# Kernel tuning notes

Measured on AMD Instinct MI355X. Metric: run time of the kernel, lower is better.

The kernel has to match this reference:

```python
import jax, jax.numpy as jnp
import numpy as np

N, L, N_KNOTS = 512, 64, 9
N_BINS = N_KNOTS - 1
TWO_PI = 2.0 * np.pi


def _circular_conv(x, w, b):
    # x: (N,C,H,W), w: (O,C,3,3); circular (periodic) padding as used for gauge lattices
    xp = jnp.pad(x, ((0, 0), (0, 0), (1, 1), (1, 1)), mode='wrap')
    y = jax.lax.conv_general_dilated(xp, w, (1, 1), 'VALID',
                                     dimension_numbers=('NCHW', 'OIHW', 'NCHW'))
    return y + b[None, :, None, None]


def setup_inputs() -> dict:
    key = jax.random.key(0)
    k1, k2, k3 = jax.random.split(key, 3)
    x = jax.random.normal(k1, (N, L, L), dtype=jnp.float32)
    # partition the lattice into active/passive/frozen masks
    pat = (np.add.outer(np.arange(L), 2 * np.arange(L)) % 3)
    mask_active = jnp.asarray((pat == 0).astype(np.float32))
    mask_passive = jnp.asarray((pat == 1).astype(np.float32))
    mask_frozen = jnp.asarray((pat == 2).astype(np.float32))
    conv1_w = 0.1 * jax.random.normal(k2, (32, 2, 3, 3), dtype=jnp.float32)
    conv1_b = jnp.zeros((32,), jnp.float32)
    conv2_w = 0.1 * jax.random.normal(k3, (3 * N_BINS + 1, 32, 3, 3), dtype=jnp.float32)
    conv2_b = jnp.zeros((3 * N_BINS + 1,), jnp.float32)
    return {"x": x, "mask_active": mask_active, "mask_passive": mask_passive,
            "mask_frozen": mask_frozen, "conv1_w": conv1_w, "conv1_b": conv1_b,
            "conv2_w": conv2_w, "conv2_b": conv2_b}


def reference(x, mask_active, mask_passive, mask_frozen, conv1_w, conv1_b, conv2_w, conv2_b):
    nb = N_BINS
    # prepare_u1_input: frozen-masked (cos, sin) channels
    net_in = mask_frozen[None, None] * jnp.stack([jnp.cos(x), jnp.sin(x)], axis=1)  # (N,2,L,L)
    h1 = jax.nn.gelu(_circular_conv(net_in, conv1_w, conv1_b))
    net_out = _circular_conv(h1, conv2_w, conv2_b)              # (N,3nb+1,L,L)
    net_out = jnp.transpose(net_out, (0, 2, 3, 1))              # (N,L,L,3nb+1)
    w = jax.nn.softmax(net_out[..., :nb], axis=-1)
    h = jax.nn.softmax(net_out[..., nb:2 * nb], axis=-1)
    d = jax.nn.softplus(net_out[..., 2 * nb:3 * nb])
    t = net_out[..., -1]
    # circular knots on [0, 2pi]; periodic derivative: s[-1] = s[0]
    zeros = jnp.zeros(w.shape[:-1] + (1,), w.dtype)
    kx = jnp.concatenate([zeros, TWO_PI * jnp.cumsum(w, -1)], -1)   # (N,L,L,n_knots)
    ky = jnp.concatenate([zeros, TWO_PI * jnp.cumsum(h, -1)], -1)
    s = jnp.concatenate([d, d[..., :1]], -1)
    # dir = 0 (forward): x1 = active * mod(x)
    x1 = mask_active[None] * jnp.remainder(x, TWO_PI)
    # bin search over interior knots -> k in [0, nb-1]
    k = jnp.sum((x1[..., None] >= kx[..., 1:-1]).astype(jnp.int32), axis=-1)
    g = lambda a, i: jnp.take_along_axis(a, i[..., None], axis=-1)[..., 0]
    kxk, kxk1 = g(kx, k), g(kx, k + 1)
    kyk, kyk1 = g(ky, k), g(ky, k + 1)
    sk, sk1 = g(s, k), g(s, k + 1)
    wk = kxk1 - kxk
    hk = kyk1 - kyk
    slope = hk / wk
    xi = jnp.clip((x1 - kxk) / wk, 0.0, 1.0)
    om = 1.0 - xi
    # rational-quadratic spline (Durkan et al. 2019)
    den = slope + (sk1 + sk - 2.0 * slope) * xi * om
    y = kyk + hk * (slope * xi * xi + sk * xi * om) / den
    local_logJ = jnp.log(slope * slope * (sk1 * xi * xi + 2.0 * slope * xi * om + sk * om * om)) \
                 - 2.0 * jnp.log(den)
    fx1 = mask_active[None] * (y + t)              # (1-dir)*t with dir=0
    local_logJ = mask_active[None] * local_logJ
    logJ = jnp.sum(local_logJ, axis=(1, 2))
    fx = mask_active[None] * jnp.remainder(fx1, TWO_PI) + mask_passive[None] * x + mask_frozen[None] * x
    return fx, logJ
```

## Files before the change

kernel.cpp:

```cpp
#include <hip/hip_runtime.h>
#include <math.h>

#define Nn 512
#define Ld 64
#define NB 8
#define C1 32
#define C2 25
#define CHUNK 8

#define ICOLS 68
#define ISTR  69
#define IROWSMAX 16
#define HCOLS 66
#define HSTR  67
#define HPLANE 945

__device__ __forceinline__ float gelu_tanh(float a) {
    float a3 = a * a * a;
    float t = tanhf(0.7978845608028654f * (a + 0.044715f * a3));
    return 0.5f * a * (1.0f + t);
}

__device__ __forceinline__ float softplus_f(float v) {
    return (v > 0.0f) ? v + log1pf(expf(-v)) : log1pf(expf(v));
}

__device__ __forceinline__ float pos_mod_2pi(float v) {
    const float T = 6.2831853071795864769f;
    float r = fmodf(v, T);
    if (r < 0.0f) r += T;
    return r;
}

__global__ __launch_bounds__(256, 4) void csplaq_v4_kernel(
    const float* __restrict__ x,
    const float* __restrict__ c1w, const float* __restrict__ c1b,
    const float* __restrict__ c2w, const float* __restrict__ c2b,
    float* __restrict__ out_fx, float* __restrict__ out_logJ)
{
    __shared__ float s_cos[IROWSMAX * ISTR];
    __shared__ float s_sin[IROWSMAX * ISTR];
    __shared__ float s_h1[CHUNK * HPLANE];
    __shared__ float s_red[4];

    const float TWO_PI_F = 6.2831853071795864769f;

    const int tid  = threadIdx.x;
    const int band = blockIdx.x;
    const int n    = blockIdx.y;
    const int r0   = band * 12;
    const int R    = (band == 5) ? 4 : 12;
    const int rows_in  = R + 4;
    const int nsite_h  = (R + 2) * HCOLS;
    const int n_active = (R == 12) ? 256 : 86;
    const float* xn = x + n * Ld * Ld;

    for (int idx = tid; idx < rows_in * ICOLS; idx += 256) {
        int li = idx / ICOLS, uu = idx - li * ICOLS;
        int gi = (r0 - 2 + li) & 63;
        int gj = (uu - 2) & 63;
        float xv = xn[gi * Ld + gj];
        int pat = (gi + 2 * gj) % 3;
        float sv, cv;
        sincosf(xv, &sv, &cv);
        float fz = (pat == 2) ? 1.0f : 0.0f;
        s_cos[li * ISTR + uu] = fz * cv;
        s_sin[li * ISTR + uu] = fz * sv;
    }

    int g3 = tid >> 6, u = tid & 63;
    int rsel  = (u >= 22) + (u >= 43);
    int ubase = (rsel == 2) ? 43 : ((rsel == 1) ? 22 : 0);
    int rr = 3 * g3 + rsel;
    int cc = 3 * (u - ubase) + rsel;
    bool is_act = (tid < n_active);

    float acc[C2];
    #pragma unroll
    for (int co = 0; co < C2; ++co) acc[co] = c2b[co];

    for (int c0 = 0; c0 < C1; c0 += CHUNK) {
        __syncthreads();
        for (int s = tid; s < nsite_h; s += 256) {
            int h = s / HCOLS, j = s - h * HCOLS;
            float v[18];
            #pragma unroll
            for (int di = 0; di < 3; ++di)
                #pragma unroll
                for (int dj = 0; dj < 3; ++dj) {
                    int a = (h + di) * ISTR + (j + dj);
                    v[di * 3 + dj]     = s_cos[a];
                    v[9 + di * 3 + dj] = s_sin[a];
                }
            #pragma unroll
            for (int c = 0; c < CHUNK; ++c) {
                const float* w = c1w + (c0 + c) * 18;
                float a1 = c1b[c0 + c];
                #pragma unroll
                for (int t = 0; t < 9; ++t) {
                    a1 = fmaf(v[t],     w[t],     a1);
                    a1 = fmaf(v[9 + t], w[9 + t], a1);
                }
                s_h1[c * HPLANE + h * HSTR + j] = gelu_tanh(a1);
            }
        }
        __syncthreads();
        if (is_act) {
            #pragma unroll 1
            for (int c = 0; c < CHUNK; ++c) {
                int ci = c0 + c;
                float v[9];
                const float* hp = s_h1 + c * HPLANE + rr * HSTR + cc;
                #pragma unroll
                for (int di = 0; di < 3; ++di)
                    #pragma unroll
                    for (int dj = 0; dj < 3; ++dj)
                        v[di * 3 + dj] = hp[di * HSTR + dj];
                const float* wp = c2w + ci * 9;
                #pragma unroll
                for (int co = 0; co < C2; ++co) {
                    const float* w = wp + co * (C1 * 9);
                    float a2 = acc[co];
                    #pragma unroll
                    for (int t = 0; t < 9; ++t) a2 = fmaf(v[t], w[t], a2);
                    acc[co] = a2;
                }
            }
        }
    }

    float* outn = out_fx + n * Ld * Ld;
    for (int idx = tid; idx < R * 64; idx += 256) {
        int lr = idx >> 6, c = idx & 63;
        int gi = r0 + lr;
        int pat = (gi + 2 * c) % 3;
        float xv = xn[gi * Ld + c];
        if (pat != 0) outn[gi * Ld + c] = xv;
    }

    float lj_val = 0.0f;
    if (is_act) {
        int gi = r0 + rr;
        float xv = xn[gi * Ld + cc];

        float kx[NB + 1], ky[NB + 1], sar[NB + 1];
        {
            float m = acc[0];
            #pragma unroll
            for (int q = 1; q < NB; ++q) m = fmaxf(m, acc[q]);
            float e[NB], ssum = 0.0f;
            #pragma unroll
            for (int q = 0; q < NB; ++q) { e[q] = expf(acc[q] - m); ssum += e[q]; }
            float inv = TWO_PI_F / ssum;
            float run = 0.0f;
            kx[0] = 0.0f;
            #pragma unroll
            for (int q = 0; q < NB; ++q) { run += e[q]; kx[q + 1] = run * inv; }
        }
        {
            float m = acc[NB];
            #pragma unroll
            for (int q = 1; q < NB; ++q) m = fmaxf(m, acc[NB + q]);
            float e[NB], ssum = 0.0f;
            #pragma unroll
            for (int q = 0; q < NB; ++q) { e[q] = expf(acc[NB + q] - m); ssum += e[q]; }
            float inv = TWO_PI_F / ssum;
            float run = 0.0f;
            ky[0] = 0.0f;
            #pragma unroll
            for (int q = 0; q < NB; ++q) { run += e[q]; ky[q + 1] = run * inv; }
        }
        #pragma unroll
        for (int q = 0; q < NB; ++q) sar[q] = softplus_f(acc[2 * NB + q]);
        sar[NB] = sar[0];
        float t_out = acc[3 * NB];

        float x1 = pos_mod_2pi(xv);
        int k = 0;
        #pragma unroll
        for (int q = 1; q <= NB - 1; ++q) k += (x1 >= kx[q]) ? 1 : 0;

        float kxk = 0.f, kxk1 = 0.f, kyk = 0.f, kyk1 = 0.f, sk = 0.f, sk1 = 0.f;
        #pragma unroll
        for (int q = 0; q <= NB; ++q) {
            if (q == k)     { kxk = kx[q];  kyk = ky[q];  sk  = sar[q]; }
            if (q == k + 1) { kxk1 = kx[q]; kyk1 = ky[q]; sk1 = sar[q]; }
        }

        float wk = kxk1 - kxk;
        float hk = kyk1 - kyk;
        float slope = hk / wk;
        float xi = (x1 - kxk) / wk;
        xi = fminf(fmaxf(xi, 0.0f), 1.0f);
        float om = 1.0f - xi;
        float den = slope + (sk1 + sk - 2.0f * slope) * xi * om;
        float y = kyk + hk * (slope * xi * xi + sk * xi * om) / den;
        float num = slope * slope * (sk1 * xi * xi + 2.0f * slope * xi * om + sk * om * om);
        lj_val = logf(num) - 2.0f * logf(den);

        outn[gi * Ld + cc] = pos_mod_2pi(y + t_out);
    }

    float r = lj_val;
    #pragma unroll
    for (int off = 32; off > 0; off >>= 1) r += __shfl_down(r, off, 64);
    int lane = tid & 63, wv = tid >> 6;
    if (lane == 0) s_red[wv] = r;
    __syncthreads();
    if (tid == 0)
        atomicAdd(&out_logJ[n], s_red[0] + s_red[1] + s_red[2] + s_red[3]);
}

extern "C" void kernel_launch(void* const* d_in, const int* in_sizes, int n_in,
                              void* d_out, int out_size, void* d_ws, size_t ws_size,
                              hipStream_t stream) {
    const float* x   = (const float*)d_in[0];
    const float* c1w = (const float*)d_in[4];
    const float* c1b = (const float*)d_in[5];
    const float* c2w = (const float*)d_in[6];
    const float* c2b = (const float*)d_in[7];

    float* out_fx   = (float*)d_out;
    float* out_logJ = out_fx + (size_t)Nn * Ld * Ld;

    hipMemsetAsync(out_logJ, 0, Nn * sizeof(float), stream);

    dim3 grid(6, Nn);
    csplaq_v4_kernel<<<grid, 256, 0, stream>>>(x, c1w, c1b, c2w, c2b, out_fx, out_logJ);
}
```

Before: 440.2 us.

## Split fused conv pipeline into conv1 kernel writing h1 to workspace plus conv2/spline kernel

Splits the single fused kernel in two. The first kernel computes conv1 plus GELU for every site once and writes all 32 channels to a global workspace. The second loads h1 tiles with float4 reads and runs conv2 and the spline. This removes the halo recomputation of conv1 in each band and lets both kernels run at higher occupancy, at the cost of a 256 MB h1 round trip through HBM. The old fused kernel remains as a fallback when the workspace is too small.

```diff
diff --git a/kernel.cpp b/kernel.cpp
--- a/kernel.cpp
+++ b/kernel.cpp
@@ -6,31 +6,240 @@
 #define NB 8
 #define C1 32
 #define C2 25
+
+__device__ __forceinline__ float gelu_tanh(float a) {
+    float a3 = a * a * a;
+    float t = tanhf(0.7978845608028654f * (a + 0.044715f * a3));
+    return 0.5f * a * (1.0f + t);
+}
+
+__device__ __forceinline__ float softplus_f(float v) {
+    return (v > 0.0f) ? v + log1pf(expf(-v)) : log1pf(expf(v));
+}
+
+__device__ __forceinline__ float pos_mod_2pi(float v) {
+    const float T = 6.2831853071795864769f;
+    float r = fmodf(v, T);
+    if (r < 0.0f) r += T;
+    return r;
+}
+
+__global__ __launch_bounds__(256, 8) void k1_conv1_kernel(
+    const float* __restrict__ x,
+    const float* __restrict__ c1w, const float* __restrict__ c1b,
+    float* __restrict__ h1g)
+{
+    __shared__ float s_cos[8 * 69];
+    __shared__ float s_sin[8 * 69];
+
+    const int tid = threadIdx.x;
+    const int rb  = blockIdx.x;
+    const int n   = blockIdx.y;
+    const int r0k = rb * 4;
+    const float* xn = x + n * 4096;
+
+    for (int idx = tid; idx < 8 * 68; idx += 256) {
+        int li = idx / 68, lj = idx - li * 68;
+        int gi = (r0k - 2 + li) & 63;
+        int gj = (lj - 2) & 63;
+        float xv = xn[gi * 64 + gj];
+        int pat = (gi + 2 * gj) % 3;
+        float sv, cv;
+        sincosf(xv, &sv, &cv);
+        float fz = (pat == 2) ? 1.0f : 0.0f;
+        s_cos[li * 69 + lj] = fz * cv;
+        s_sin[li * 69 + lj] = fz * sv;
+    }
+    __syncthreads();
+
+    const int gj = tid & 63, lrow = tid >> 6;
+    const int gi = r0k + lrow;
+
+    float v[18];
+    #pragma unroll
+    for (int di = 0; di < 3; ++di)
+        #pragma unroll
+        for (int dj = 0; dj < 3; ++dj) {
+            int a = (lrow + 1 + di) * 69 + (gj + 1 + dj);
+            v[di * 3 + dj]     = s_cos[a];
+            v[9 + di * 3 + dj] = s_sin[a];
+        }
+
+    float* outp = h1g + (size_t)n * C1 * 4096 + gi * 64 + gj;
+    #pragma unroll 4
+    for (int c = 0; c < C1; ++c) {
+        const float* w = c1w + c * 18;
+        float a1 = c1b[c];
+        #pragma unroll
+        for (int t = 0; t < 9; ++t) {
+            a1 = fmaf(v[t],     w[t],     a1);
+            a1 = fmaf(v[9 + t], w[9 + t], a1);
+        }
+        outp[(size_t)c * 4096] = gelu_tanh(a1);
+    }
+}
+
+#define K2CH 4
+#define K2PLANE (14 * 64)
+
+__global__ __launch_bounds__(256, 8) void k2_conv2_spline_kernel(
+    const float* __restrict__ x, const float* __restrict__ h1g,
+    const float* __restrict__ c2w, const float* __restrict__ c2b,
+    float* __restrict__ out_fx, float* __restrict__ out_logJ)
+{
+    __shared__ float s_h1[K2CH * K2PLANE];
+    __shared__ float s_red[4];
+
+    const float TWO_PI_F = 6.2831853071795864769f;
+
+    const int tid  = threadIdx.x;
+    const int band = blockIdx.x;
+    const int n    = blockIdx.y;
+    const int r0   = band * 12;
+    const int R    = (band == 5) ? 4 : 12;
+    const int rows_l   = R + 2;
+    const int n_active = (R == 12) ? 256 : 86;
+    const float* xn  = x + n * 4096;
+    const float* h1n = h1g + (size_t)n * C1 * 4096;
+
+    int g3 = tid >> 6, u = tid & 63;
+    int rsel  = (u >= 22) + (u >= 43);
+    int ubase = (rsel == 2) ? 43 : ((rsel == 1) ? 22 : 0);
+    int rr = 3 * g3 + rsel;
+    int cc = 3 * (u - ubase) + rsel;
+    bool is_act = (tid < n_active);
+    int jm = (cc + 63) & 63, jp = (cc + 1) & 63;
+
+    float acc[C2];
+    #pragma unroll
+    for (int co = 0; co < C2; ++co) acc[co] = c2b[co];
+
+    for (int c0 = 0; c0 < C1; c0 += K2CH) {
+        __syncthreads();
+        int nf4 = K2CH * rows_l * 16;
+        for (int f = tid; f < nf4; f += 256) {
+            int c   = f / (rows_l * 16);
+            int rem = f - c * (rows_l * 16);
+            int r = rem >> 4, cg = rem & 15;
+            int grow = (r0 - 1 + r) & 63;
+            float4 src = *(const float4*)(h1n + (size_t)(c0 + c) * 4096 + grow * 64 + cg * 4);
+            *(float4*)(&s_h1[c * K2PLANE + r * 64 + cg * 4]) = src;
+        }
+        __syncthreads();
+        if (is_act) {
+            #pragma unroll 1
+            for (int c = 0; c < K2CH; ++c) {
+                int ci = c0 + c;
+                float v[9];
+                #pragma unroll
+                for (int di = 0; di < 3; ++di) {
+                    const float* rowp = s_h1 + c * K2PLANE + (rr + di) * 64;
+                    v[di * 3 + 0] = rowp[jm];
+                    v[di * 3 + 1] = rowp[cc];
+                    v[di * 3 + 2] = rowp[jp];
+                }
+                const float* wp = c2w + ci * 9;
+                #pragma unroll
+                for (int co = 0; co < C2; ++co) {
+                    const float* w = wp + co * (C1 * 9);
+                    float a2 = acc[co];
+                    #pragma unroll
+                    for (int t = 0; t < 9; ++t) a2 = fmaf(v[t], w[t], a2);
+                    acc[co] = a2;
+                }
+            }
+        }
+    }
+
+    float* outn = out_fx + n * 4096;
+    for (int idx = tid; idx < R * 64; idx += 256) {
+        int lr = idx >> 6, c = idx & 63;
+        int gi = r0 + lr;
+        int pat = (gi + 2 * c) % 3;
+        float xv = xn[gi * 64 + c];
+        if (pat != 0) outn[gi * 64 + c] = xv;
+    }
+
+    float lj_val = 0.0f;
+    if (is_act) {
+        int gi = r0 + rr;
+        float xv = xn[gi * 64 + cc];
+
+        float kx[NB + 1], ky[NB + 1], sar[NB + 1];
+        {
+            float m = acc[0];
+            #pragma unroll
+            for (int q = 1; q < NB; ++q) m = fmaxf(m, acc[q]);
+            float e[NB], ssum = 0.0f;
+            #pragma unroll
+            for (int q = 0; q < NB; ++q) { e[q] = expf(acc[q] - m); ssum += e[q]; }
+            float inv = TWO_PI_F / ssum;
+            float run = 0.0f;
+            kx[0] = 0.0f;
+            #pragma unroll
+            for (int q = 0; q < NB; ++q) { run += e[q]; kx[q + 1] = run * inv; }
+        }
+        {
+            float m = acc[NB];
+            #pragma unroll
+            for (int q = 1; q < NB; ++q) m = fmaxf(m, acc[NB + q]);
+            float e[NB], ssum = 0.0f;
+            #pragma unroll
+            for (int q = 0; q < NB; ++q) { e[q] = expf(acc[NB + q] - m); ssum += e[q]; }
+            float inv = TWO_PI_F / ssum;
+            float run = 0.0f;
+            ky[0] = 0.0f;
+            #pragma unroll
+            for (int q = 0; q < NB; ++q) { run += e[q]; ky[q + 1] = run * inv; }
+        }
+        #pragma unroll
+        for (int q = 0; q < NB; ++q) sar[q] = softplus_f(acc[2 * NB + q]);
+        sar[NB] = sar[0];
+        float t_out = acc[3 * NB];
+
+        float x1 = pos_mod_2pi(xv);
+        int k = 0;
+        #pragma unroll
+        for (int q = 1; q <= NB - 1; ++q) k += (x1 >= kx[q]) ? 1 : 0;
+
+        float kxk = 0.f, kxk1 = 0.f, kyk = 0.f, kyk1 = 0.f, sk = 0.f, sk1 = 0.f;
+        #pragma unroll
+        for (int q = 0; q <= NB; ++q) {
+            if (q == k)     { kxk = kx[q];  kyk = ky[q];  sk  = sar[q]; }
+            if (q == k + 1) { kxk1 = kx[q]; kyk1 = ky[q]; sk1 = sar[q]; }
+        }
+
+        float wk = kxk1 - kxk;
+        float hk = kyk1 - kyk;
+        float slope = hk / wk;
+        float xi = (x1 - kxk) / wk;
+        xi = fminf(fmaxf(xi, 0.0f), 1.0f);
+        float om = 1.0f - xi;
+        float den = slope + (sk1 + sk - 2.0f * slope) * xi * om;
+        float y = kyk + hk * (slope * xi * xi + sk * xi * om) / den;
+        float num = slope * slope * (sk1 * xi * xi + 2.0f * slope * xi * om + sk * om * om);
+        lj_val = logf(num) - 2.0f * logf(den);
+
+        outn[gi * 64 + cc] = pos_mod_2pi(y + t_out);
+    }
+
+    float r = lj_val;
+    #pragma unroll
+    for (int off = 32; off > 0; off >>= 1) r += __shfl_down(r, off, 64);
+    int lane = tid & 63, wv = tid >> 6;
+    if (lane == 0) s_red[wv] = r;
+    __syncthreads();
+    if (tid == 0)
+        atomicAdd(&out_logJ[n], s_red[0] + s_red[1] + s_red[2] + s_red[3]);
+}
+
 #define CHUNK 8
-
 #define ICOLS 68
 #define ISTR  69
 #define IROWSMAX 16
 #define HCOLS 66
 #define HSTR  67
 #define HPLANE 945
-
-__device__ __forceinline__ float gelu_tanh(float a) {
-    float a3 = a * a * a;
-    float t = tanhf(0.7978845608028654f * (a + 0.044715f * a3));
-    return 0.5f * a * (1.0f + t);
-}
-
-__device__ __forceinline__ float softplus_f(float v) {
-    return (v > 0.0f) ? v + log1pf(expf(-v)) : log1pf(expf(v));
-}
-
-__device__ __forceinline__ float pos_mod_2pi(float v) {
-    const float T = 6.2831853071795864769f;
-    float r = fmodf(v, T);
-    if (r < 0.0f) r += T;
-    return r;
-}
 
 __global__ __launch_bounds__(256, 4) void csplaq_v4_kernel(
     const float* __restrict__ x,
@@ -44,7 +253,6 @@
     __shared__ float s_red[4];
 
     const float TWO_PI_F = 6.2831853071795864769f;
-
     const int tid  = threadIdx.x;
     const int band = blockIdx.x;
     const int n    = blockIdx.y;
@@ -142,7 +350,6 @@
     if (is_act) {
         int gi = r0 + rr;
         float xv = xn[gi * Ld + cc];
-
         float kx[NB + 1], ky[NB + 1], sar[NB + 1];
         {
             float m = acc[0];
@@ -225,6 +432,15 @@
 
     hipMemsetAsync(out_logJ, 0, Nn * sizeof(float), stream);
 
-    dim3 grid(6, Nn);
-    csplaq_v4_kernel<<<grid, 256, 0, stream>>>(x, c1w, c1b, c2w, c2b, out_fx, out_logJ);
-}
+    const size_t h1_bytes = (size_t)Nn * C1 * Ld * Ld * sizeof(float);
+    if (ws_size >= h1_bytes) {
+        float* h1g = (float*)d_ws;
+        dim3 g1(16, Nn);
+        k1_conv1_kernel<<<g1, 256, 0, stream>>>(x, c1w, c1b, h1g);
+        dim3 g2(6, Nn);
+        k2_conv2_spline_kernel<<<g2, 256, 0, stream>>>(x, h1g, c2w, c2b, out_fx, out_logJ);
+    } else {
+        dim3 grid(6, Nn);
+        csplaq_v4_kernel<<<grid, 256, 0, stream>>>(x, c1w, c1b, c2w, c2b, out_fx, out_logJ);
+    }
+}
```

Measured after the change: 396.7 us. 1.11x faster.
